# Performance work log

Measured on AMD Instinct MI355X. Metric: run time of the kernel, lower is better.

Reference implementation:

```python
import jax, jax.numpy as jnp
import numpy as np

N, C, W = 16, 512, 4096          # batch lines, channels, max width (frames)
FINAL_DIM = 512
MASK_WIDTH = 4
NUM_NEGATIVES = 10
NUM_MASKS = 256                  # ~ mask_prob * T_total / mask_width


def _build_static():
    # Deterministic ragged lengths, already descending (pack_padded_sequence order).
    seq_len = (W - 128 * np.arange(N)).astype(np.int64)       # [4096, 3968, ..., 2176]
    t = np.arange(W)[:, None]                                  # time-major outer axis
    b = np.arange(N)[None, :]
    valid = seq_len[None, :] > t                               # [W, N]
    # pack_padded_sequence layout: for each t, all batches with len>t (desc length order)
    pack_idx = ((b * W + t)[valid]).astype(np.int64)           # [T_total] indices into flat (N*W)
    T = pack_idx.shape[0]                                      # 50176
    n_blocks = T // MASK_WIDTH
    rng = np.random.default_rng(0)
    perm = rng.permutation(n_blocks)
    sel1 = np.sort(perm[:NUM_MASKS])
    sel2 = np.sort(perm[NUM_MASKS:NUM_MASKS + NUM_NEGATIVES * NUM_MASKS])
    off = np.arange(MASK_WIDTH)
    # non-overlapping contiguous mask_width blocks, ascending (boolean-mask gather order)
    masked_idx = (sel1[:, None] * MASK_WIDTH + off).ravel().astype(np.int64)   # mask == 1
    neg_idx = (sel2[:, None] * MASK_WIDTH + off).ravel().astype(np.int64)      # mask == 2
    return seq_len, pack_idx, masked_idx, neg_idx


def setup_inputs() -> dict:
    key = jax.random.key(0)
    k1, k2, k3 = jax.random.split(key, 3)
    seq_len, pack_idx, masked_idx, neg_idx = _build_static()
    inputs = jax.random.normal(k1, (N, C, 1, W), dtype=jnp.float32)
    mask_emb = jax.random.normal(k2, (MASK_WIDTH, C), dtype=jnp.float32) * 0.02
    Wq = jax.random.normal(k3, (FINAL_DIM, C), dtype=jnp.float32) * (1.0 / np.sqrt(C))
    bq = jnp.zeros((FINAL_DIM,), dtype=jnp.float32)
    return {
        'inputs': inputs,
        'seq_len': jnp.asarray(seq_len, jnp.int32),
        'pack_idx': jnp.asarray(pack_idx, jnp.int32),
        'masked_idx': jnp.asarray(masked_idx, jnp.int32),
        'neg_idx': jnp.asarray(neg_idx, jnp.int32),
        'mask_emb': mask_emb,
        'Wq': Wq,
        'bq': bq,
    }


def reference(inputs, seq_len, pack_idx, masked_idx, neg_idx, mask_emb, Wq, bq):
    Nn, Cc, H, Ww = inputs.shape                              # H == 1
    # (N, C, 1, W) -> (N, W, 1, C) -> flat (N*W, C)
    x = jnp.transpose(inputs, (0, 3, 2, 1)).reshape(Nn * Ww, Cc)
    packed = x[pack_idx]                                      # [T_total, C] packed (time-major)
    # project_q on masked (mask==1) and negative (mask==2) token groups
    unmasked = (packed[masked_idx] @ Wq.T + bq).reshape(1, NUM_MASKS, MASK_WIDTH, FINAL_DIM)
    negatives = (packed[neg_idx] @ Wq.T + bq).reshape(NUM_NEGATIVES, NUM_MASKS, MASK_WIDTH, FINAL_DIM)
    # overwrite masked positions with the repeated mask embedding table
    packed = packed.at[masked_idx].set(jnp.tile(mask_emb, (NUM_MASKS, 1)))
    # pad_packed_sequence: scatter back to padded (N, W, C), zeros elsewhere
    out = jnp.zeros((Nn * Ww, Cc), dtype=inputs.dtype).at[pack_idx].set(packed)
    out = out.reshape(Nn, Ww, Cc).transpose(0, 2, 1)[:, :, None, :]   # (N, C, 1, W)
    return out, unmasked, negatives
```

## Files before the change

kernel.cpp:

```cpp
#include <hip/hip_runtime.h>

#define NB 16
#define CC 512
#define WW 4096
#define FD 512
#define NMASK 1024
#define T_COMB 11264
#define OUT0_ELEMS (NB*CC*WW)

#define WS_LOOKUP_OFF 0
#define WS_WQ_OFF     262144
#define WS_A_OFF      786432

#define S_LDS 36

typedef __attribute__((ext_vector_type(8))) short short8;
typedef __attribute__((ext_vector_type(4))) float f32x4;

__device__ __forceinline__ unsigned short f2bf(float x) {
  unsigned int u = __builtin_bit_cast(unsigned int, x);
  u += 0x7fffu + ((u >> 16) & 1u);
  return (unsigned short)(u >> 16);
}

__device__ __forceinline__ void gload_lds16(const void* gp, void* lp) {
  __builtin_amdgcn_global_load_lds(
      (__attribute__((address_space(1))) void*)(gp),
      (__attribute__((address_space(3))) void*)(lp),
      16, 0, 0);
}

__global__ __launch_bounds__(256) void scatter_lookup_k(
    const int* __restrict__ pack_idx, const int* __restrict__ masked_idx,
    const int* __restrict__ neg_idx, int* __restrict__ lookup) {
  int g = blockIdx.x * 256 + threadIdx.x;
  int pidx = (g < NMASK) ? masked_idx[g] : neg_idx[g - NMASK];
  lookup[pack_idx[pidx]] = g;
}

__global__ __launch_bounds__(256) void fused_copy_k(
    const float* __restrict__ in, const int* __restrict__ seq_len,
    const int* __restrict__ lookup, const float* __restrict__ mask_emb,
    const float* __restrict__ Wq, float* __restrict__ out0,
    unsigned short* __restrict__ A_ws, unsigned short* __restrict__ Wq_ws) {
  if (blockIdx.x >= 2048) {
    int b2 = blockIdx.x - 2048;
    const float4* wq4 = (const float4*)Wq;
    for (int it = 0; it < 4; ++it) {
      int i4 = it * 16384 + b2 * 256 + (int)threadIdx.x;
      float4 v = wq4[i4];
      ushort4 o;
      o.x = f2bf(v.x); o.y = f2bf(v.y); o.z = f2bf(v.z); o.w = f2bf(v.w);
      ((ushort4*)Wq_ws)[i4] = o;
    }
    return;
  }
  __shared__ unsigned short tile[CC * S_LDS];
  __shared__ int g_s[32];
  const int tid = threadIdx.x;
  const int bx = blockIdx.x;
  const int n = bx >> 7;
  const int w0 = (bx & 127) * 32;
  if (tid < 32) g_s[tid] = lookup[n * WW + w0 + tid];

  const int wl4 = (tid & 7) * 4;
  const int w = w0 + wl4;
  const int4 g4 = *(const int4*)&lookup[n * WW + w];
  const int L = seq_len[n];
  const int gg[4] = {g4.x, g4.y, g4.z, g4.w};

  const float4* in4 = (const float4*)in;
  float4* out4 = (float4*)out0;
  const size_t rowbase = ((size_t)n << 21) + (size_t)w;

#pragma unroll 4
  for (int it = 0; it < 16; ++it) {
    int c = it * 32 + (tid >> 3);
    size_t e = rowbase + ((size_t)c << 12);
    float4 v = in4[e >> 2];
    float vv[4] = {v.x, v.y, v.z, v.w};
    ushort4 bf;
    bf.x = f2bf(vv[0]); bf.y = f2bf(vv[1]); bf.z = f2bf(vv[2]); bf.w = f2bf(vv[3]);
    *(ushort4*)&tile[c * S_LDS + wl4] = bf;
    float o[4];
#pragma unroll
    for (int k = 0; k < 4; ++k) {
      float val = (w + k < L) ? vv[k] : 0.0f;
      int g = gg[k];
      if ((unsigned)g < (unsigned)NMASK) val = mask_emb[(g & 3) * CC + c];
      o[k] = val;
    }
    float4 ov = {o[0], o[1], o[2], o[3]};
    out4[e >> 2] = ov;
  }
  __syncthreads();

  const int c2 = tid * 2;
  for (int wl = 0; wl < 32; ++wl) {
    int g = g_s[wl];
    if (g < 0) continue;
    ushort2 val;
    val.x = tile[c2 * S_LDS + wl];
    val.y = tile[(c2 + 1) * S_LDS + wl];
    *(ushort2*)&A_ws[(size_t)g * CC + c2] = val;
  }
}

__global__ __launch_bounds__(256) void gemm_k(
    const unsigned short* __restrict__ A, const unsigned short* __restrict__ B,
    const float* __restrict__ bq, float* __restrict__ out) {
  __shared__ unsigned short As[128 * 32];
  __shared__ unsigned short Bs[128 * 32];
  const int tid = threadIdx.x;
  const int lane = tid & 63;
  const int quad = lane >> 4;
  const int r16 = lane & 15;
  const int wv = tid >> 6;
  const int bm = blockIdx.x * 128;
  const int bf = blockIdx.y * 128;
  const int wm = (wv & 1) * 64;
  const int wf = (wv >> 1) * 64;
  const int wbase = tid & ~63;

  f32x4 acc[4][4];
#pragma unroll
  for (int mi = 0; mi < 4; ++mi)
#pragma unroll
    for (int fi = 0; fi < 4; ++fi)
      acc[mi][fi] = (f32x4){0.f, 0.f, 0.f, 0.f};

  for (int k0 = 0; k0 < 512; k0 += 32) {
#pragma unroll
    for (int it = 0; it < 2; ++it) {
      int ch = it * 256 + tid;
      int row = ch >> 2;
      int cg = ch & 3;
      int ubase = (it * 256 + wbase) * 8;
      gload_lds16(A + (size_t)(bm + row) * 512 + k0 + cg * 8, &As[ubase]);
      gload_lds16(B + (size_t)(bf + row) * 512 + k0 + cg * 8, &Bs[ubase]);
    }
    asm volatile("s_waitcnt vmcnt(0)" ::: "memory");
    __syncthreads();

    short8 a[4], b[4];
#pragma unroll
    for (int mi = 0; mi < 4; ++mi)
      a[mi] = *(const short8*)&As[(wm + mi * 16 + r16) * 32 + quad * 8];
#pragma unroll
    for (int fi = 0; fi < 4; ++fi)
      b[fi] = *(const short8*)&Bs[(wf + fi * 16 + r16) * 32 + quad * 8];
#pragma unroll
    for (int mi = 0; mi < 4; ++mi)
#pragma unroll
      for (int fi = 0; fi < 4; ++fi)
        acc[mi][fi] = __builtin_amdgcn_mfma_f32_16x16x32_bf16(
            a[mi], b[fi], acc[mi][fi], 0, 0, 0);
    __syncthreads();
  }

#pragma unroll
  for (int fi = 0; fi < 4; ++fi) {
    int f = bf + wf + fi * 16 + r16;
    float bqv = bq[f];
#pragma unroll
    for (int mi = 0; mi < 4; ++mi) {
      int m0 = bm + wm + mi * 16 + quad * 4;
#pragma unroll
      for (int r = 0; r < 4; ++r)
        out[(size_t)(m0 + r) * 512 + f] = acc[mi][fi][r] + bqv;
    }
  }
}

extern "C" void kernel_launch(void* const* d_in, const int* in_sizes, int n_in,
                              void* d_out, int out_size, void* d_ws, size_t ws_size,
                              hipStream_t stream) {
  const float* inputs    = (const float*)d_in[0];
  const int*   seq_len   = (const int*)d_in[1];
  const int*   pack_idx  = (const int*)d_in[2];
  const int*   masked_idx= (const int*)d_in[3];
  const int*   neg_idx   = (const int*)d_in[4];
  const float* mask_emb  = (const float*)d_in[5];
  const float* Wq        = (const float*)d_in[6];
  const float* bq        = (const float*)d_in[7];
  float* out = (float*)d_out;
  char* ws = (char*)d_ws;
  int* lookup = (int*)(ws + WS_LOOKUP_OFF);
  unsigned short* wqb = (unsigned short*)(ws + WS_WQ_OFF);
  unsigned short* aws = (unsigned short*)(ws + WS_A_OFF);

  hipMemsetAsync(lookup, 0xFF, NB * WW * sizeof(int), stream);
  scatter_lookup_k<<<44, 256, 0, stream>>>(pack_idx, masked_idx, neg_idx, lookup);
  fused_copy_k<<<2112, 256, 0, stream>>>(inputs, seq_len, lookup, mask_emb, Wq,
                                         out, aws, wqb);
  gemm_k<<<dim3(88, 4), 256, 0, stream>>>(aws, wqb, bq, out + OUT0_ELEMS);
}
```

Baseline: 300.7 us.

## Skip input reads for padded tiles, branch masks by wavefront, and retile the GEMM

The copy kernel now detects 32-frame tiles lying entirely past the sequence length. For those tiles it writes zeros and exits, skipping the input load, the bf16 tile staging and the lookup reads. For valid tiles it drops the per-element length check and uses a wavefront ballot to skip mask-embedding substitution when no lane holds a masked column. The gather loop now visits only selected columns through a ballot bitmask. The GEMM block tile shrinks from 128x128 to 64x128, doubling the grid for better occupancy at the cost of reloading each B tile more often.

```diff
diff --git a/kernel.cpp b/kernel.cpp
--- a/kernel.cpp
+++ b/kernel.cpp
@@ -46,6 +46,7 @@
   if (blockIdx.x >= 2048) {
     int b2 = blockIdx.x - 2048;
     const float4* wq4 = (const float4*)Wq;
+#pragma unroll
     for (int it = 0; it < 4; ++it) {
       int i4 = it * 16384 + b2 * 256 + (int)threadIdx.x;
       float4 v = wq4[i4];
@@ -55,50 +56,68 @@
     }
     return;
   }
-  __shared__ unsigned short tile[CC * S_LDS];
-  __shared__ int g_s[32];
   const int tid = threadIdx.x;
   const int bx = blockIdx.x;
   const int n = bx >> 7;
   const int w0 = (bx & 127) * 32;
-  if (tid < 32) g_s[tid] = lookup[n * WW + w0 + tid];
-
   const int wl4 = (tid & 7) * 4;
   const int w = w0 + wl4;
+  const int c0 = tid >> 3;
+  const size_t rowbase = ((size_t)n << 21) + (size_t)w;
+  float4* out4 = (float4*)out0;
+  const int L = seq_len[n];
+
+  if (w0 + 32 > L) {
+    float4 z = {0.f, 0.f, 0.f, 0.f};
+#pragma unroll
+    for (int it = 0; it < 16; ++it) {
+      int c = it * 32 + c0;
+      out4[(rowbase + ((size_t)c << 12)) >> 2] = z;
+    }
+    return;
+  }
+
+  __shared__ unsigned short tile[CC * S_LDS];
+  __shared__ int g_s[32];
+  if (tid < 32) g_s[tid] = lookup[n * WW + w0 + tid];
+
   const int4 g4 = *(const int4*)&lookup[n * WW + w];
-  const int L = seq_len[n];
   const int gg[4] = {g4.x, g4.y, g4.z, g4.w};
+  bool lane_has_mask = ((unsigned)gg[0] < (unsigned)NMASK) |
+                       ((unsigned)gg[1] < (unsigned)NMASK) |
+                       ((unsigned)gg[2] < (unsigned)NMASK) |
+                       ((unsigned)gg[3] < (unsigned)NMASK);
+  bool has_mask = __ballot(lane_has_mask) != 0ull;
 
   const float4* in4 = (const float4*)in;
-  float4* out4 = (float4*)out0;
-  const size_t rowbase = ((size_t)n << 21) + (size_t)w;
-
-#pragma unroll 4
+#pragma unroll
   for (int it = 0; it < 16; ++it) {
-    int c = it * 32 + (tid >> 3);
-    size_t e = rowbase + ((size_t)c << 12);
-    float4 v = in4[e >> 2];
-    float vv[4] = {v.x, v.y, v.z, v.w};
+    int c = it * 32 + c0;
+    size_t i4 = (rowbase + ((size_t)c << 12)) >> 2;
+    float4 v = in4[i4];
     ushort4 bf;
-    bf.x = f2bf(vv[0]); bf.y = f2bf(vv[1]); bf.z = f2bf(vv[2]); bf.w = f2bf(vv[3]);
+    bf.x = f2bf(v.x); bf.y = f2bf(v.y); bf.z = f2bf(v.z); bf.w = f2bf(v.w);
     *(ushort4*)&tile[c * S_LDS + wl4] = bf;
-    float o[4];
-#pragma unroll
-    for (int k = 0; k < 4; ++k) {
-      float val = (w + k < L) ? vv[k] : 0.0f;
-      int g = gg[k];
-      if ((unsigned)g < (unsigned)NMASK) val = mask_emb[(g & 3) * CC + c];
-      o[k] = val;
-    }
-    float4 ov = {o[0], o[1], o[2], o[3]};
-    out4[e >> 2] = ov;
+    if (has_mask) {
+      float o[4] = {v.x, v.y, v.z, v.w};
+#pragma unroll
+      for (int k = 0; k < 4; ++k)
+        if ((unsigned)gg[k] < (unsigned)NMASK)
+          o[k] = mask_emb[(gg[k] & 3) * CC + c];
+      v.x = o[0]; v.y = o[1]; v.z = o[2]; v.w = o[3];
+    }
+    out4[i4] = v;
   }
   __syncthreads();
 
+  const int lane = tid & 63;
+  bool sel = (lane < 32) && (g_s[lane & 31] >= 0);
+  unsigned smask = (unsigned)__ballot(sel);
   const int c2 = tid * 2;
-  for (int wl = 0; wl < 32; ++wl) {
+  while (smask) {
+    int wl = __builtin_ctz(smask);
+    smask &= smask - 1;
     int g = g_s[wl];
-    if (g < 0) continue;
     ushort2 val;
     val.x = tile[c2 * S_LDS + wl];
     val.y = tile[(c2 + 1) * S_LDS + wl];
@@ -109,48 +128,50 @@
 __global__ __launch_bounds__(256) void gemm_k(
     const unsigned short* __restrict__ A, const unsigned short* __restrict__ B,
     const float* __restrict__ bq, float* __restrict__ out) {
-  __shared__ unsigned short As[128 * 32];
+  __shared__ unsigned short As[64 * 32];
   __shared__ unsigned short Bs[128 * 32];
   const int tid = threadIdx.x;
   const int lane = tid & 63;
   const int quad = lane >> 4;
   const int r16 = lane & 15;
   const int wv = tid >> 6;
-  const int bm = blockIdx.x * 128;
+  const int bm = blockIdx.x * 64;
   const int bf = blockIdx.y * 128;
-  const int wm = (wv & 1) * 64;
+  const int wm = (wv & 1) * 32;
   const int wf = (wv >> 1) * 64;
   const int wbase = tid & ~63;
 
-  f32x4 acc[4][4];
-#pragma unroll
-  for (int mi = 0; mi < 4; ++mi)
+  f32x4 acc[2][4];
+#pragma unroll
+  for (int mi = 0; mi < 2; ++mi)
 #pragma unroll
     for (int fi = 0; fi < 4; ++fi)
       acc[mi][fi] = (f32x4){0.f, 0.f, 0.f, 0.f};
 
   for (int k0 = 0; k0 < 512; k0 += 32) {
+    {
+      int row = tid >> 2, cg = tid & 3;
+      gload_lds16(A + (size_t)(bm + row) * 512 + k0 + cg * 8, &As[wbase * 8]);
+    }
 #pragma unroll
     for (int it = 0; it < 2; ++it) {
       int ch = it * 256 + tid;
-      int row = ch >> 2;
-      int cg = ch & 3;
-      int ubase = (it * 256 + wbase) * 8;
-      gload_lds16(A + (size_t)(bm + row) * 512 + k0 + cg * 8, &As[ubase]);
-      gload_lds16(B + (size_t)(bf + row) * 512 + k0 + cg * 8, &Bs[ubase]);
+      int row = ch >> 2, cg = ch & 3;
+      gload_lds16(B + (size_t)(bf + row) * 512 + k0 + cg * 8,
+                  &Bs[(it * 256 + wbase) * 8]);
     }
     asm volatile("s_waitcnt vmcnt(0)" ::: "memory");
     __syncthreads();
 
-    short8 a[4], b[4];
-#pragma unroll
-    for (int mi = 0; mi < 4; ++mi)
+    short8 a[2], b[4];
+#pragma unroll
+    for (int mi = 0; mi < 2; ++mi)
       a[mi] = *(const short8*)&As[(wm + mi * 16 + r16) * 32 + quad * 8];
 #pragma unroll
     for (int fi = 0; fi < 4; ++fi)
       b[fi] = *(const short8*)&Bs[(wf + fi * 16 + r16) * 32 + quad * 8];
 #pragma unroll
-    for (int mi = 0; mi < 4; ++mi)
+    for (int mi = 0; mi < 2; ++mi)
 #pragma unroll
       for (int fi = 0; fi < 4; ++fi)
         acc[mi][fi] = __builtin_amdgcn_mfma_f32_16x16x32_bf16(
@@ -163,7 +184,7 @@
     int f = bf + wf + fi * 16 + r16;
     float bqv = bq[f];
 #pragma unroll
-    for (int mi = 0; mi < 4; ++mi) {
+    for (int mi = 0; mi < 2; ++mi) {
       int m0 = bm + wm + mi * 16 + quad * 4;
 #pragma unroll
       for (int r = 0; r < 4; ++r)
@@ -193,5 +214,5 @@
   scatter_lookup_k<<<44, 256, 0, stream>>>(pack_idx, masked_idx, neg_idx, lookup);
   fused_copy_k<<<2112, 256, 0, stream>>>(inputs, seq_len, lookup, mask_emb, Wq,
                                          out, aws, wqb);
-  gemm_k<<<dim3(88, 4), 256, 0, stream>>>(aws, wqb, bq, out + OUT0_ELEMS);
-}
+  gemm_k<<<dim3(176, 4), 256, 0, stream>>>(aws, wqb, bq, out + OUT0_ELEMS);
+}
```

Result: no change. 296.1 us (-1.5%).
